# Optimization experiments

Hardware: AMD Instinct MI355X
Metric: run time of the kernel (lower is better)

The kernel has to match this reference:

```python
import jax, jax.numpy as jnp
import numpy as np

MAX_FPS = 30.0
NUM_HEADS = 8


def _rope(x, times):
    # x: [B, H, T, D] with D even; interleaved rotary (even/odd pairs)
    B, H, T, D = x.shape
    inv_freq = 1.0 / (10000.0 ** (jnp.arange(0, D, 2, dtype=jnp.float32) / D))  # [D/2]
    pos = jnp.round(times * MAX_FPS)                       # [B, T]
    freqs = pos[:, :, None] * inv_freq[None, None, :]      # [B, T, D/2]
    cos = jnp.cos(freqs)[:, None, :, :]                    # [B, 1, T, D/2]
    sin = jnp.sin(freqs)[:, None, :, :]
    xp = x.reshape(B, H, T, D // 2, 2)
    x0, x1 = xp[..., 0], xp[..., 1]                        # even-index, odd-index elems
    r0 = x0 * cos - x1 * sin
    r1 = x0 * sin + x1 * cos
    return jnp.stack([r0, r1], axis=-1).reshape(B, H, T, D)


def setup_inputs() -> dict:
    key = jax.random.key(0)
    k1, k2, k3, k4, k5 = jax.random.split(key, 5)
    B, N, C = 4, 2048, 512
    x = jax.random.normal(k1, (B, N, C), dtype=jnp.float32)
    mask = jnp.zeros((B, N), dtype=jnp.float32)  # additive mask, 0 = attend
    # times in seconds; rounded to frame indices inside RoPE
    times = jax.random.uniform(k2, (B, N), dtype=jnp.float32) * (N / MAX_FPS)
    bound_qkv = float(np.sqrt(6.0 / (C + 3 * C)))
    Wqkv = jax.random.uniform(k3, (3 * C, C), minval=-bound_qkv, maxval=bound_qkv, dtype=jnp.float32)
    bound_p = float(np.sqrt(6.0 / (C + C)))
    Wproj = jax.random.uniform(k4, (C, C), minval=-bound_p, maxval=bound_p, dtype=jnp.float32)
    bproj = jnp.zeros((C,), dtype=jnp.float32)
    return {"x": x, "mask": mask, "times": times, "Wqkv": Wqkv,
            "Wproj": Wproj, "bproj": bproj, "num_cls_token": 0}


def reference(x, mask, times, Wqkv, Wproj, bproj, num_cls_token):
    B, N, C = x.shape
    H = NUM_HEADS
    Dh = C // H
    qkv = (x @ Wqkv.T).reshape(B, N, 3, H, Dh).transpose(2, 0, 3, 1, 4)  # [3,B,H,N,Dh]
    q, k, v = qkv[0], qkv[1], qkv[2]
    if num_cls_token > 0:
        c_q, q = q[:, :, :num_cls_token], q[:, :, num_cls_token:]
        c_k, k = k[:, :, :num_cls_token], k[:, :, num_cls_token:]
        t = times
        q = _rope(q, t)
        k = _rope(k, t)
        q = jnp.concatenate([c_q, q], axis=2)
        k = jnp.concatenate([c_k, k], axis=2)
    else:
        q = _rope(q, times)
        k = _rope(k, times)
    scale = 1.0 / jnp.sqrt(jnp.float32(Dh))
    scores = jnp.einsum('bhqd,bhkd->bhqk', q, k) * scale + mask[:, None, None, :]
    attn = jax.nn.softmax(scores, axis=-1)
    out = jnp.einsum('bhqk,bhkd->bhqd', attn, v)           # [B,H,N,Dh]
    out = out.transpose(0, 2, 1, 3).reshape(B, N, C)
    return out @ Wproj.T + bproj
```

## Files before the change

kernel.cpp:

```cpp
#include <hip/hip_runtime.h>
#include <math.h>

#define BB 4
#define NN 2048
#define CC 512
#define HH 8
#define DH 64
#define MM (BB*NN)
#define QKV_N (3*CC)
#define NSP 2
#define SLICE ((size_t)32 * NN)

typedef _Float16 f16;
typedef __attribute__((ext_vector_type(2))) _Float16 f16x2;
typedef __attribute__((ext_vector_type(4))) _Float16 f16x4;
typedef __attribute__((ext_vector_type(8))) _Float16 f16x8;
typedef __attribute__((ext_vector_type(4))) float f32x4;
typedef __attribute__((ext_vector_type(2))) __fp16 h16x2;

#define L2E 1.4426950408889634f
#define QSCL (0.125f * L2E)

__device__ __forceinline__ float fast_exp2(float x) {
#if __has_builtin(__builtin_amdgcn_exp2f)
    return __builtin_amdgcn_exp2f(x);
#else
    float r;
    asm volatile("v_exp_f32 %0, %1\n\ts_nop 1" : "=v"(r) : "v"(x));
    return r;
#endif
}

#define GL16(g, l) __builtin_amdgcn_global_load_lds(                       \
    (const __attribute__((address_space(1))) void*)(g),                    \
    (__attribute__((address_space(3))) void*)(l), 16, 0, 0)

#define SX4 (MM*CC/4)
#define SW4 (QKV_N*CC/4)
#define SP4 (CC*CC/4)
#define CAST_T (SX4 + SW4 + SP4)
#define TAB_T (MM * 32)
#define WT_T  (MM / 8)
__global__ __launch_bounds__(256) void cast_tab_kernel(
    const float* __restrict__ x, const float* __restrict__ wqkv,
    const float* __restrict__ wproj, const float* __restrict__ times,
    const float* __restrict__ mask,
    f16* __restrict__ xh, f16* __restrict__ wqh, f16* __restrict__ wph,
    float2* __restrict__ tab, f16* __restrict__ wtab)
{
    const int t = blockIdx.x * 256 + threadIdx.x;
    if (t < CAST_T) {
        const float* src; f16* dst; int i;
        bool qscale = false;
        if (t < SX4)            { src = x;     dst = xh;  i = t; }
        else if (t < SX4 + SW4) { src = wqkv;  dst = wqh; i = t - SX4;
                                  qscale = (i < CC*CC/4); }
        else                    { src = wproj; dst = wph; i = t - SX4 - SW4; }
        f32x4 v = *(const f32x4*)(src + 4 * (size_t)i);
        if (qscale) v *= QSCL;
        f16x4 h = { (f16)v[0], (f16)v[1], (f16)v[2], (f16)v[3] };
        *(f16x4*)(dst + 4 * (size_t)i) = h;
    } else if (t < CAST_T + TAB_T) {
        const int idx = t - CAST_T;
        const int row = idx >> 5, fi = idx & 31;
        const float pos = rintf(times[row] * 30.0f);
        const float invf = exp2f((float)fi * (-13.287712379549449f / 32.0f));
        float s, c;
        sincosf(pos * invf, &s, &c);
        tab[idx] = make_float2(c, s);
    } else {
        const int i = t - CAST_T - TAB_T;
        f32x4 m0 = *(const f32x4*)(mask + 8 * (size_t)i);
        f32x4 m1 = *(const f32x4*)(mask + 8 * (size_t)i + 4);
        f16x8 wv;
        #pragma unroll
        for (int r = 0; r < 4; ++r) {
            wv[r]     = (f16)fast_exp2(m0[r] * L2E);
            wv[4 + r] = (f16)fast_exp2(m1[r] * L2E);
        }
        *(f16x8*)(wtab + 8 * (size_t)i) = wv;
    }
}

__global__ __launch_bounds__(256) void qkv_gemm(
    const f16* __restrict__ xh, const f16* __restrict__ wh,
    const float2* __restrict__ tab, const int* __restrict__ nclsp,
    const f16* __restrict__ wtab,
    f16* __restrict__ qo, f16* __restrict__ ksw, f16* __restrict__ vsw)
{
    __shared__ __align__(16) char smem[16896];
    f16 (*As)[32] = (f16 (*)[32])smem;
    f16 (*Bs)[32] = (f16 (*)[32])(smem + 8192);

    const int m0 = blockIdx.x * 128;
    const int n0 = blockIdx.y * 128;
    const int tid = threadIdx.x;
    const int lane = tid & 63;
    const int w = tid >> 6;
    const int wm = (w & 1) * 64, wn = (w >> 1) * 64;
    const int l15 = lane & 15, quad = lane >> 4;

    const int sr = tid >> 2;
    const int sc = (tid & 3) * 8;
    const f16* ga0 = xh + (size_t)(m0 + sr) * CC + sc;
    const f16* ga1 = xh + (size_t)(m0 + sr + 64) * CC + sc;
    const f16* gb0 = wh + (size_t)(n0 + sr) * CC + sc;
    const f16* gb1 = wh + (size_t)(n0 + sr + 64) * CC + sc;
    f16* la0 = &As[sr][sc];      f16* la1 = &As[sr + 64][sc];
    f16* lb0 = &Bs[sr][sc];      f16* lb1 = &Bs[sr + 64][sc];

    f32x4 acc[4][4] = {};
    for (int k0 = 0; k0 < CC; k0 += 32) {
        __syncthreads();
        GL16(ga0 + k0, la0);
        GL16(ga1 + k0, la1);
        GL16(gb0 + k0, lb0);
        GL16(gb1 + k0, lb1);
        __syncthreads();

        f16x8 af[4], bf[4];
        #pragma unroll
        for (int mi = 0; mi < 4; ++mi)
            af[mi] = *(const f16x8*)&As[wm + mi*16 + l15][quad * 8];
        #pragma unroll
        for (int ni = 0; ni < 4; ++ni)
            bf[ni] = *(const f16x8*)&Bs[wn + ni*16 + l15][quad * 8];
        #pragma unroll
        for (int mi = 0; mi < 4; ++mi)
            #pragma unroll
            for (int ni = 0; ni < 4; ++ni)
                acc[mi][ni] = __builtin_amdgcn_mfma_f32_16x16x32_f16(
                    af[mi], bf[ni], acc[mi][ni], 0, 0, 0);
    }
    __syncthreads();

    const int which = n0 >> 9;
    const int b     = m0 >> 11;
    const int mloc  = m0 & (NN - 1);
    const int hbase = (n0 & 511) >> 6;

    if (which < 2) {
        f16 (*Tr)[132] = (f16 (*)[132])smem;
        const int ncls = *nclsp;
        #pragma unroll
        for (int c = 0; c < 2; ++c) {
            if ((w & 1) == c) {
                #pragma unroll
                for (int mi = 0; mi < 4; ++mi)
                    #pragma unroll
                    for (int ni = 0; ni < 4; ++ni)
                        #pragma unroll
                        for (int r = 0; r < 4; ++r)
                            Tr[16*mi + quad*4 + r][wn + 16*ni + l15] =
                                (f16)acc[mi][ni][r];
            }
            __syncthreads();
            const int row = tid >> 2, cg = tid & 3;
            const int n   = mloc + c*64 + row;
            const int hh  = hbase + (cg >> 1);
            const int d0  = (cg & 1) * 32;
            f16x8 vv[4];
            #pragma unroll
            for (int j = 0; j < 4; ++j)
                vv[j] = *(const f16x8*)&Tr[row][cg*32 + j*8];
            if (n >= ncls) {
                const f32x4* t4 = (const f32x4*)(tab + ((size_t)b*NN + n)*32
                                                 + (d0 >> 1));
                #pragma unroll
                for (int j = 0; j < 4; ++j) {
                    f32x4 cs0 = t4[2*j];
                    f32x4 cs1 = t4[2*j + 1];
                    #pragma unroll
                    for (int p = 0; p < 4; ++p) {
                        const float co = (p < 2) ? cs0[(p & 1)*2]
                                                 : cs1[(p & 1)*2];
                        const float s  = (p < 2) ? cs0[(p & 1)*2 + 1]
                                                 : cs1[(p & 1)*2 + 1];
                        const float x0 = (float)vv[j][2*p];
                        const float x1 = (float)vv[j][2*p+1];
                        vv[j][2*p]   = (f16)(x0*co - x1*s);
                        vv[j][2*p+1] = (f16)(x0*s + x1*co);
                    }
                }
            }
            if (which == 0) {
                f16* qp = qo + (((size_t)(b*HH + hh))*NN + n)*DH + d0;
                #pragma unroll
                for (int j = 0; j < 4; ++j)
                    *(f16x8*)(qp + 8*j) = vv[j];
            } else {
                const int ktile = (mloc >> 6) + c;
                f16* kp = ksw + ((((size_t)(b*HH + hh))*32 + ktile)*64 + row)*64;
                #pragma unroll
                for (int j = 0; j < 4; ++j) {
                    const int blk = (d0 >> 3) + j;
                    *(f16x8*)(kp + ((blk ^ (row & 7)) * 8)) = vv[j];
                }
            }
            if (c == 0) __syncthreads();
        }
        return;
    }

    f16 (*Tv)[66] = (f16 (*)[66])smem;
    #pragma unroll
    for (int c = 0; c < 2; ++c) {
        if ((w & 1) == c) {
            #pragma unroll
            for (int mi = 0; mi < 4; ++mi)
                #pragma unroll
                for (int ni = 0; ni < 4; ++ni) {
                    f16x4 pk = { (f16)acc[mi][ni][0], (f16)acc[mi][ni][1],
                                 (f16)acc[mi][ni][2], (f16)acc[mi][ni][3] };
                    *(f16x4*)&Tv[wn + 16*ni + l15][16*mi + quad*4] = pk;
                }
        }
        __syncthreads();
        const int rr = tid >> 1;
        const int d  = rr & 63, hh = hbase + (rr >> 6);
        const int ktile = (mloc >> 6) + c;
        f16* vp = vsw + ((((size_t)(b*HH + hh))*32 + ktile)*64 + d)*64;
        #pragma unroll
        for (int j = 0; j < 4; ++j) {
            const int blk = (tid & 1)*4 + j;
            f16x8 t = *(const f16x8*)&Tv[rr][(tid & 1)*32 + j*8];
            t *= *(const f16x8*)&wtab[(size_t)b*NN + mloc + c*64
                                      + (tid & 1)*32 + j*8];
            *(f16x8*)(vp + ((blk ^ (d & 7)) * 8)) = t;
        }
        if (c == 0) __syncthreads();
    }
}

__global__ __launch_bounds__(256, 4) void attn_kernel(
    const f16* __restrict__ qg, const f16* __restrict__ ksw,
    const f16* __restrict__ vsw, const f16* __restrict__ wtab,
    f16* __restrict__ On, float* __restrict__ lbuf)
{
    __shared__ __align__(16) f16 asm_[4][4096];

    const int bh = blockIdx.x, qt = blockIdx.y, sp = blockIdx.z;
    const int b = bh >> 3;
    const int tid = threadIdx.x;
    const int w = tid >> 6, lane = tid & 63;
    const int l15 = lane & 15, quad = lane >> 4;
    const int rho = l15 & 7;

    const f16* qbase = qg + ((size_t)bh * NN + qt*128 + w*32) * DH;
    const f16* kt0 = ksw + ((size_t)bh * 32 + sp*16) * 4096;
    const f16* vt0 = vsw + ((size_t)bh * 32 + sp*16) * 4096;
    const f16* wsl = wtab + (size_t)b * NN + sp*1024;

    f16x8 Bq[2][2];
    #pragma unroll
    for (int ni = 0; ni < 2; ++ni)
        #pragma unroll
        for (int kc = 0; kc < 2; ++kc)
            Bq[ni][kc] = *(const f16x8*)(qbase + (size_t)(16*ni + l15) * DH
                                         + kc*32 + quad*8);

    const f16x4 zf4 = {};
    const f32x4 fz = {};
    f32x4 O[2][4] = {};
    f32x4 Lacc[2] = {};

    {
        const f16* ks = kt0 + tid*8;
        const f16* vs = vt0 + tid*8;
        GL16(ks,        &asm_[0][tid*8]);
        GL16(ks + 2048, &asm_[0][2048 + tid*8]);
        GL16(vs,        &asm_[1][tid*8]);
        GL16(vs + 2048, &asm_[1][2048 + tid*8]);
    }

    for (int kt = 0; kt < 16; ++kt) {
        const int cur = (kt & 1) * 2;
        __syncthreads();
        if (kt + 1 < 16) {
            const int nxt = 2 - cur;
            const f16* ks = kt0 + (size_t)(kt+1)*4096 + tid*8;
            const f16* vs = vt0 + (size_t)(kt+1)*4096 + tid*8;
            GL16(ks,        &asm_[nxt][tid*8]);
            GL16(ks + 2048, &asm_[nxt][2048 + tid*8]);
            GL16(vs,        &asm_[nxt+1][tid*8]);
            GL16(vs + 2048, &asm_[nxt+1][2048 + tid*8]);
        }
        const f16 (*Kh)[64] = (const f16 (*)[64])asm_[cur];
        const f16 (*Vt)[64] = (const f16 (*)[64])asm_[cur + 1];

        f16x4 Aw[4];
        #pragma unroll
        for (int mi = 0; mi < 4; ++mi) {
            f16x4 wv = *(const f16x4*)(wsl + kt*64 + 16*mi + quad*4);
            Aw[mi] = (l15 == 0) ? wv : zf4;
        }

        f32x4 st[4][2];
        const int aw = (quad ^ rho) * 8;
        #pragma unroll
        for (int mi = 0; mi < 4; ++mi) {
            f16x8 Ak0 = *(const f16x8*)&Kh[16*mi + l15][aw];
            f16x8 Ak1 = *(const f16x8*)&Kh[16*mi + l15][aw ^ 32];
            #pragma unroll
            for (int ni = 0; ni < 2; ++ni) {
                f32x4 t0 = __builtin_amdgcn_mfma_f32_16x16x32_f16(
                    Ak0, Bq[ni][0], fz, 0, 0, 0);
                st[mi][ni] = __builtin_amdgcn_mfma_f32_16x16x32_f16(
                    Ak1, Bq[ni][1], t0, 0, 0, 0);
            }
        }

        f16x4 ph[4][2];
        #pragma unroll
        for (int ni = 0; ni < 2; ++ni)
            #pragma unroll
            for (int mi = 0; mi < 4; ++mi) {
                float e0 = fast_exp2(st[mi][ni][0]);
                float e1 = fast_exp2(st[mi][ni][1]);
                float e2 = fast_exp2(st[mi][ni][2]);
                float e3 = fast_exp2(st[mi][ni][3]);
                h16x2 lo = __builtin_amdgcn_cvt_pkrtz(e0, e1);
                h16x2 hi = __builtin_amdgcn_cvt_pkrtz(e2, e3);
                f16x2 lo2 = __builtin_bit_cast(f16x2, lo);
                f16x2 hi2 = __builtin_bit_cast(f16x2, hi);
                ph[mi][ni] = __builtin_shufflevector(lo2, hi2, 0, 1, 2, 3);
            }

        #pragma unroll
        for (int mi = 0; mi < 4; ++mi) {
            Lacc[0] = __builtin_amdgcn_mfma_f32_16x16x16f16(Aw[mi], ph[mi][0], Lacc[0], 0, 0, 0);
            Lacc[1] = __builtin_amdgcn_mfma_f32_16x16x16f16(Aw[mi], ph[mi][1], Lacc[1], 0, 0, 0);
            #pragma unroll
            for (int nd = 0; nd < 4; ++nd) {
                const int vb = ((2*mi + (quad >> 1)) ^ rho) * 8 + (quad & 1) * 4;
                f16x4 Av = *(const f16x4*)&Vt[16*nd + l15][vb];
                O[0][nd] = __builtin_amdgcn_mfma_f32_16x16x16f16(Av, ph[mi][0], O[0][nd], 0, 0, 0);
                O[1][nd] = __builtin_amdgcn_mfma_f32_16x16x16f16(Av, ph[mi][1], O[1][nd], 0, 0, 0);
            }
        }
    }

    #pragma unroll
    for (int ni = 0; ni < 2; ++ni) {
        const float l = __shfl(Lacc[ni][0], l15);
        const float inv = 1.0f / l;
        const int qrow = qt*128 + w*32 + 16*ni + l15;
        const size_t rbase = (size_t)sp * SLICE + (size_t)bh * NN + qrow;
        f16* obase = On + rbase * DH;
        #pragma unroll
        for (int nd = 0; nd < 4; ++nd) {
            f32x4 o = O[ni][nd] * inv;
            f16x4 oh = { (f16)o[0], (f16)o[1], (f16)o[2], (f16)o[3] };
            *(f16x4*)(obase + 16*nd + quad*4) = oh;
        }
        if (quad == 0)
            lbuf[rbase] = l;
    }
}

__global__ __launch_bounds__(256) void proj_gemm(
    const f16* __restrict__ On, const float* __restrict__ lbuf,
    const f16* __restrict__ wh, const float* __restrict__ bias,
    float* __restrict__ out)
{
    __shared__ f16 As[128][32];
    __shared__ f16 Bs[64][32];
    const int m0 = blockIdx.x * 128;
    const int n0 = blockIdx.y * 64;
    const int tid = threadIdx.x;
    const int lane = tid & 63;
    const int w = tid >> 6;
    const int wm = (w & 1) * 64, wn = (w >> 1) * 32;
    const int l15 = lane & 15, quad = lane >> 4;

    const int b  = m0 >> 11;
    const int q0 = m0 & (NN - 1);

    const int sr = tid >> 2;
    const int sc = (tid & 3) * 8;
    const f16* gb0 = wh + (size_t)(n0 + sr) * CC + sc;
    f16* lb0 = &Bs[sr][sc];

    f32x4 acc[4][2] = {};
    for (int k0 = 0; k0 < CC; k0 += 32) {
        const int h  = k0 >> 6;
        const int d0 = k0 & 63;
        __syncthreads();
        GL16(gb0 + k0, lb0);
        const size_t row0 = (size_t)(b*HH + h) * NN + q0 + sr;
        #pragma unroll
        for (int rr = 0; rr < 2; ++rr) {
            const size_t row = row0 + rr*64;
            const float l0 = lbuf[row], l1 = lbuf[SLICE + row];
            const float inv = 1.0f / (l0 + l1);
            const float w0 = l0 * inv, w1 = l1 * inv;
            f16x8 a0 = *(const f16x8*)(On + row * DH + d0 + sc);
            f16x8 a1 = *(const f16x8*)(On + (SLICE + row) * DH + d0 + sc);
            f16x8 o;
            #pragma unroll
            for (int r = 0; r < 8; ++r)
                o[r] = (f16)(w0 * (float)a0[r] + w1 * (float)a1[r]);
            *(f16x8*)&As[sr + rr*64][sc] = o;
        }
        __syncthreads();

        f16x8 af[4], bf[2];
        #pragma unroll
        for (int mi = 0; mi < 4; ++mi)
            af[mi] = *(const f16x8*)&As[wm + mi*16 + l15][quad * 8];
        #pragma unroll
        for (int ni = 0; ni < 2; ++ni)
            bf[ni] = *(const f16x8*)&Bs[wn + ni*16 + l15][quad * 8];
        #pragma unroll
        for (int mi = 0; mi < 4; ++mi)
            #pragma unroll
            for (int ni = 0; ni < 2; ++ni)
                acc[mi][ni] = __builtin_amdgcn_mfma_f32_16x16x32_f16(
                    af[mi], bf[ni], acc[mi][ni], 0, 0, 0);
    }

    float bb[2];
    #pragma unroll
    for (int ni = 0; ni < 2; ++ni)
        bb[ni] = bias[n0 + wn + ni*16 + l15];

    #pragma unroll
    for (int mi = 0; mi < 4; ++mi)
        #pragma unroll
        for (int r = 0; r < 4; ++r) {
            const int m = m0 + wm + mi*16 + quad*4 + r;
            #pragma unroll
            for (int ni = 0; ni < 2; ++ni)
                out[(size_t)m * CC + n0 + wn + ni*16 + l15] = acc[mi][ni][r] + bb[ni];
        }
}

extern "C" void kernel_launch(void* const* d_in, const int* in_sizes, int n_in,
                              void* d_out, int out_size, void* d_ws, size_t ws_size,
                              hipStream_t stream)
{
    const float* x     = (const float*)d_in[0];
    const float* mask  = (const float*)d_in[1];
    const float* times = (const float*)d_in[2];
    const float* Wqkv  = (const float*)d_in[3];
    const float* Wproj = (const float*)d_in[4];
    const float* bproj = (const float*)d_in[5];
    const int*   ncls  = (const int*)d_in[6];
    float* out = (float*)d_out;

    const size_t per = (size_t)BB * HH * NN * DH;
    f16* xh  = (f16*)d_ws;
    f16* wqh = xh + per;
    f16* wph = wqh + (size_t)QKV_N * CC;
    f16* q   = wph + (size_t)CC * CC;
    f16* ks  = q + per;
    f16* vs  = ks + per;
    f16* On  = vs + per;
    float* lb = (float*)(On + NSP * per);
    float2* tab = (float2*)(lb + NSP * 32 * NN);
    f16* wtab = (f16*)(tab + (size_t)MM * 32);

    cast_tab_kernel<<<(CAST_T + TAB_T + WT_T) / 256, 256, 0, stream>>>(
        x, Wqkv, Wproj, times, mask, xh, wqh, wph, tab, wtab);
    qkv_gemm<<<dim3(MM / 128, QKV_N / 128), 256, 0, stream>>>(
        xh, wqh, tab, ncls, wtab, q, ks, vs);
    attn_kernel<<<dim3(BB * HH, NN / 128, NSP), 256, 0, stream>>>(
        q, ks, vs, wtab, On, lb);
    proj_gemm<<<dim3(MM / 128, CC / 64), 256, 0, stream>>>(
        On, lb, wph, bproj, out);
}
```

Measured before the change: 174.8 us.

## Use 16x16x32 MFMA for PV, compute row sums with fdot2, add setprio

The P·V product now pairs two 16-key blocks so it can use the wider 16x16x32 f16 MFMA, which halves the number of MFMA issues in that stage. The row-sum (L) accumulation moves off the MFMA unit to per-lane fdot2 instructions followed by a cross-quad shuffle reduction. s_setprio hints are wrapped around the MFMA phases so waves interleave matrix and exp work better. The cost is extra VALU work and more register shuffling.

Result: no change. 171.6 us (-1.8%).

```diff
diff --git a/kernel.cpp b/kernel.cpp
--- a/kernel.cpp
+++ b/kernel.cpp
@@ -28,6 +28,14 @@
     float r;
     asm volatile("v_exp_f32 %0, %1\n\ts_nop 1" : "=v"(r) : "v"(x));
     return r;
+#endif
+}
+
+__device__ __forceinline__ float fdot2(f16x2 a, f16x2 b, float c) {
+#if __has_builtin(__builtin_amdgcn_fdot2)
+    return __builtin_amdgcn_fdot2(a, b, c, false);
+#else
+    return c + (float)a[0]*(float)b[0] + (float)a[1]*(float)b[1];
 #endif
 }
 
@@ -259,10 +267,9 @@
             Bq[ni][kc] = *(const f16x8*)(qbase + (size_t)(16*ni + l15) * DH
                                          + kc*32 + quad*8);
 
-    const f16x4 zf4 = {};
     const f32x4 fz = {};
     f32x4 O[2][4] = {};
-    f32x4 Lacc[2] = {};
+    float accL[2] = {};
 
     {
         const f16* ks = kt0 + tid*8;
@@ -288,15 +295,9 @@
         const f16 (*Kh)[64] = (const f16 (*)[64])asm_[cur];
         const f16 (*Vt)[64] = (const f16 (*)[64])asm_[cur + 1];
 
-        f16x4 Aw[4];
-        #pragma unroll
-        for (int mi = 0; mi < 4; ++mi) {
-            f16x4 wv = *(const f16x4*)(wsl + kt*64 + 16*mi + quad*4);
-            Aw[mi] = (l15 == 0) ? wv : zf4;
-        }
-
         f32x4 st[4][2];
         const int aw = (quad ^ rho) * 8;
+        __builtin_amdgcn_s_setprio(1);
         #pragma unroll
         for (int mi = 0; mi < 4; ++mi) {
             f16x8 Ak0 = *(const f16x8*)&Kh[16*mi + l15][aw];
@@ -309,12 +310,13 @@
                     Ak1, Bq[ni][1], t0, 0, 0, 0);
             }
         }
+        __builtin_amdgcn_s_setprio(0);
 
         f16x4 ph[4][2];
         #pragma unroll
-        for (int ni = 0; ni < 2; ++ni)
-            #pragma unroll
-            for (int mi = 0; mi < 4; ++mi) {
+        for (int mi = 0; mi < 4; ++mi) {
+            #pragma unroll
+            for (int ni = 0; ni < 2; ++ni) {
                 float e0 = fast_exp2(st[mi][ni][0]);
                 float e1 = fast_exp2(st[mi][ni][1]);
                 float e2 = fast_exp2(st[mi][ni][2]);
@@ -325,24 +327,47 @@
                 f16x2 hi2 = __builtin_bit_cast(f16x2, hi);
                 ph[mi][ni] = __builtin_shufflevector(lo2, hi2, 0, 1, 2, 3);
             }
-
-        #pragma unroll
-        for (int mi = 0; mi < 4; ++mi) {
-            Lacc[0] = __builtin_amdgcn_mfma_f32_16x16x16f16(Aw[mi], ph[mi][0], Lacc[0], 0, 0, 0);
-            Lacc[1] = __builtin_amdgcn_mfma_f32_16x16x16f16(Aw[mi], ph[mi][1], Lacc[1], 0, 0, 0);
+            f16x4 wv = *(const f16x4*)(wsl + kt*64 + 16*mi + quad*4);
+            f16x2 wlo = __builtin_shufflevector(wv, wv, 0, 1);
+            f16x2 whi = __builtin_shufflevector(wv, wv, 2, 3);
+            #pragma unroll
+            for (int ni = 0; ni < 2; ++ni) {
+                f16x2 plo = __builtin_shufflevector(ph[mi][ni], ph[mi][ni], 0, 1);
+                f16x2 phi = __builtin_shufflevector(ph[mi][ni], ph[mi][ni], 2, 3);
+                accL[ni] = fdot2(plo, wlo, accL[ni]);
+                accL[ni] = fdot2(phi, whi, accL[ni]);
+            }
+        }
+
+        __builtin_amdgcn_s_setprio(1);
+        #pragma unroll
+        for (int g = 0; g < 2; ++g) {
+            f16x8 p0 = __builtin_shufflevector(ph[2*g][0], ph[2*g+1][0],
+                                               0, 1, 2, 3, 4, 5, 6, 7);
+            f16x8 p1 = __builtin_shufflevector(ph[2*g][1], ph[2*g+1][1],
+                                               0, 1, 2, 3, 4, 5, 6, 7);
+            const int vb1 = (((4*g + (quad >> 1)) ^ rho) * 8) + (quad & 1) * 4;
+            const int vb2 = (((4*g + 2 + (quad >> 1)) ^ rho) * 8) + (quad & 1) * 4;
             #pragma unroll
             for (int nd = 0; nd < 4; ++nd) {
-                const int vb = ((2*mi + (quad >> 1)) ^ rho) * 8 + (quad & 1) * 4;
-                f16x4 Av = *(const f16x4*)&Vt[16*nd + l15][vb];
-                O[0][nd] = __builtin_amdgcn_mfma_f32_16x16x16f16(Av, ph[mi][0], O[0][nd], 0, 0, 0);
-                O[1][nd] = __builtin_amdgcn_mfma_f32_16x16x16f16(Av, ph[mi][1], O[1][nd], 0, 0, 0);
-            }
-        }
+                f16x4 av0 = *(const f16x4*)&Vt[16*nd + l15][vb1];
+                f16x4 av1 = *(const f16x4*)&Vt[16*nd + l15][vb2];
+                f16x8 Av = __builtin_shufflevector(av0, av1,
+                                                   0, 1, 2, 3, 4, 5, 6, 7);
+                O[0][nd] = __builtin_amdgcn_mfma_f32_16x16x32_f16(
+                    Av, p0, O[0][nd], 0, 0, 0);
+                O[1][nd] = __builtin_amdgcn_mfma_f32_16x16x32_f16(
+                    Av, p1, O[1][nd], 0, 0, 0);
+            }
+        }
+        __builtin_amdgcn_s_setprio(0);
     }
 
     #pragma unroll
     for (int ni = 0; ni < 2; ++ni) {
-        const float l = __shfl(Lacc[ni][0], l15);
+        float l = accL[ni];
+        l += __shfl_xor(l, 16);
+        l += __shfl_xor(l, 32);
         const float inv = 1.0f / l;
         const int qrow = qt*128 + w*32 + 16*ni + l15;
         const size_t rbase = (size_t)sp * SLICE + (size_t)bh * NN + qrow;
```
